# Kernel tuning notes

Hardware: AMD Instinct MI355X
Metric: run time of the kernel (lower is better)

Reference implementation:

```python
import jax, jax.numpy as jnp
import numpy as np

D = 1024
H = 16
DH = D // H  # 64


def setup_inputs() -> dict:
    key = jax.random.key(0)
    ks = jax.random.split(key, 11)
    B, S = 2, 2048
    s = 1.0 / np.sqrt(D)  # torch Linear default init scale (uniform bound)
    mk = lambda k, shape: jax.random.uniform(k, shape, jnp.float32, -s, s)
    return {
        "q": jax.random.normal(ks[0], (B, S, D), jnp.float32),
        "k": jax.random.normal(ks[1], (B, S, D), jnp.float32),
        "v": jax.random.normal(ks[2], (B, S, D), jnp.float32),
        "Wq": mk(ks[3], (D, D)), "bq": mk(ks[4], (D,)),
        "Wk": mk(ks[5], (D, D)), "bk": mk(ks[6], (D,)),
        "Wv": mk(ks[7], (D, D)), "bv": mk(ks[8], (D,)),
        "Wo": mk(ks[9], (D, D)), "bo": mk(ks[10], (D,)),
    }


def reference(q, k, v, Wq, bq, Wk, bk, Wv, bv, Wo, bo):
    B, S, _ = q.shape
    scaling = DH ** (-0.5)
    # torch Linear: x @ W.T + b ; then split heads -> (B, H, S, DH)
    split = lambda x: x.reshape(B, -1, H, DH).transpose(0, 2, 1, 3)
    Q = split(q @ Wq.T + bq)
    K = split(k @ Wk.T + bk)
    V = split(v @ Wv.T + bv)
    scores = jnp.einsum("bhqd,bhkd->bhqk", Q, K) * scaling  # [B,H,S,S]
    attn = jax.nn.softmax(scores, axis=-1)
    out = jnp.einsum("bhqk,bhkd->bhqd", attn, V)
    out = out.transpose(0, 2, 1, 3).reshape(B, S, D)
    return out @ Wo.T + bo
```

## Files before the change

### kernel.cpp

```cpp
#include <hip/hip_runtime.h>
#include <stdint.h>

#define DIM   1024
#define HEADS 16
#define DHEAD 64
#define SEQ   2048
#define MROWS 4096
#define NQ    (MROWS * DIM)
#define NW    (DIM * DIM)

typedef unsigned short u16;
typedef __attribute__((ext_vector_type(8))) short short8;
typedef __attribute__((ext_vector_type(4))) float f32x4;
typedef __attribute__((ext_vector_type(16))) float f32x16;

static_assert(sizeof(short8) == 16, "short8 must be 16B");

__device__ __forceinline__ float bf2f(u16 u) {
  union { float f; uint32_t u; } x; x.u = ((uint32_t)u) << 16; return x.f;
}
__device__ __forceinline__ u16 f2bf(float f) {
  union { float f; uint32_t u; } x; x.f = f;
  uint32_t r = x.u + 0x7FFFu + ((x.u >> 16) & 1u);
  return (u16)(r >> 16);
}
__device__ __forceinline__ uint32_t cvtpk(float lo, float hi) {
  uint32_t r;
  asm("v_cvt_pk_bf16_f32 %0, %1, %2" : "=v"(r) : "v"(lo), "v"(hi));
  return r;
}
__device__ __forceinline__ float exp2fast(float x) {
#if __has_builtin(__builtin_amdgcn_exp2f)
  return __builtin_amdgcn_exp2f(x);
#else
  return __expf(x * 0.69314718055994531f);
#endif
}

#if __has_builtin(__builtin_amdgcn_global_load_lds)
#define HAVE_GLLDS 1
#else
#define HAVE_GLLDS 0
#endif

__device__ __forceinline__ void stage16(const u16* src, u16* ldsbase, int cb, int lane) {
#if HAVE_GLLDS
  (void)lane;
  __builtin_amdgcn_global_load_lds((const __attribute__((address_space(1))) void*)src,
                                   (__attribute__((address_space(3))) void*)(ldsbase + (size_t)cb * 8),
                                   16, 0, 0);
#else
  *(short8*)(ldsbase + ((size_t)cb + lane) * 8) = *(const short8*)src;
#endif
}

__global__ __launch_bounds__(256)
void cvt_all(const float* __restrict__ q, const float* __restrict__ k, const float* __restrict__ v,
             const float* __restrict__ wq, const float* __restrict__ wk,
             const float* __restrict__ wv, const float* __restrict__ wo,
             u16* __restrict__ qc, u16* __restrict__ kc, u16* __restrict__ vc,
             u16* __restrict__ wqc, u16* __restrict__ wkc, u16* __restrict__ wvc, u16* __restrict__ woc)
{
  const float* s; u16* d; int n;
  switch (blockIdx.y) {
    case 0: s = q;  d = qc;  n = NQ; break;
    case 1: s = k;  d = kc;  n = NQ; break;
    case 2: s = v;  d = vc;  n = NQ; break;
    case 3: s = wq; d = wqc; n = NW; break;
    case 4: s = wk; d = wkc; n = NW; break;
    case 5: s = wv; d = wvc; n = NW; break;
    default: s = wo; d = woc; n = NW; break;
  }
  const int n8 = n >> 3;
  for (int i = blockIdx.x * blockDim.x + threadIdx.x; i < n8; i += gridDim.x * blockDim.x) {
    float4 f0 = ((const float4*)s)[2 * i];
    float4 f1 = ((const float4*)s)[2 * i + 1];
    short8 o;
    o[0] = (short)f2bf(f0.x); o[1] = (short)f2bf(f0.y);
    o[2] = (short)f2bf(f0.z); o[3] = (short)f2bf(f0.w);
    o[4] = (short)f2bf(f1.x); o[5] = (short)f2bf(f1.y);
    o[6] = (short)f2bf(f1.z); o[7] = (short)f2bf(f1.w);
    ((short8*)d)[i] = o;
  }
}

template <int RM, int RN, int MODE>
__global__ __launch_bounds__(256)
void gemm_nt(const u16* __restrict__ A0, const u16* __restrict__ W0, const float* __restrict__ b0, void* __restrict__ O0, float s0_,
             const u16* __restrict__ A1, const u16* __restrict__ W1, const float* __restrict__ b1, void* __restrict__ O1, float s1_,
             const u16* __restrict__ A2, const u16* __restrict__ W2, const float* __restrict__ b2, void* __restrict__ O2, float s2_)
{
  constexpr int BM = 32 * RM, BN = 32 * RN, BK = 64;
  __shared__ u16 As[BM * BK];
  __shared__ u16 Bs[BN * BK];

  const u16* A = A0; const u16* W = W0; const float* bias = b0; void* O = O0; float oscale = s0_;
  if (blockIdx.z == 1) { A = A1; W = W1; bias = b1; O = O1; oscale = s1_; }
  else if (blockIdx.z == 2) { A = A2; W = W2; bias = b2; O = O2; oscale = s2_; }

  const int tid  = threadIdx.x;
  const int wave = tid >> 6, lane = tid & 63;
  const int g = lane >> 4, cc = lane & 15;
  const int wr = wave >> 1, wc = wave & 1;
  const int m0 = blockIdx.x * BM, n0 = blockIdx.y * BN;

  f32x4 acc[RM][RN];
  for (int m = 0; m < RM; ++m)
    for (int n = 0; n < RN; ++n) acc[m][n] = (f32x4){0.f, 0.f, 0.f, 0.f};

  for (int k0 = 0; k0 < DIM; k0 += BK) {
    __syncthreads();
    constexpr int AI = (BM * 8) / 256;
    for (int i = 0; i < AI; ++i) {
      int cb = (wave * AI + i) * 64;
      int ch = cb + lane;
      int row = ch >> 3, kc = ch & 7;
      stage16(A + (size_t)(m0 + row) * DIM + k0 + kc * 8, As, cb, lane);
    }
    constexpr int BI = (BN * 8) / 256;
    for (int i = 0; i < BI; ++i) {
      int cb = (wave * BI + i) * 64;
      int ch = cb + lane;
      int row = ch >> 3, kc = ch & 7;
      stage16(W + (size_t)(n0 + row) * DIM + k0 + kc * 8, Bs, cb, lane);
    }
    __syncthreads();

    for (int kk = 0; kk < 2; ++kk) {
      short8 af[RM], bfr[RN];
      for (int m = 0; m < RM; ++m)
        af[m] = *(const short8*)(As + (size_t)(wr * (16 * RM) + m * 16 + cc) * BK + kk * 32 + g * 8);
      for (int n = 0; n < RN; ++n)
        bfr[n] = *(const short8*)(Bs + (size_t)(wc * (16 * RN) + n * 16 + cc) * BK + kk * 32 + g * 8);
      for (int m = 0; m < RM; ++m)
        for (int n = 0; n < RN; ++n)
          acc[m][n] = __builtin_amdgcn_mfma_f32_16x16x32_bf16(af[m], bfr[n], acc[m][n], 0, 0, 0);
    }
  }

  for (int n = 0; n < RN; ++n) {
    int col = n0 + wc * (16 * RN) + n * 16 + cc;
    float bv = bias[col];
    for (int m = 0; m < RM; ++m) {
      int rowb = m0 + wr * (16 * RM) + m * 16 + g * 4;
      for (int r = 0; r < 4; ++r) {
        int row = rowb + r;
        float val = (acc[m][n][r] + bv) * oscale;
        if (MODE == 0) {
          int b = row >> 11, s = row & (SEQ - 1);
          int hh = col >> 6, dh = col & 63;
          ((u16*)O)[((((size_t)b * HEADS + hh) * SEQ + s) << 6) + dh] = f2bf(val);
        } else {
          ((float*)O)[(size_t)row * DIM + col] = val;
        }
      }
    }
  }
}

#if __has_builtin(__builtin_amdgcn_permlane32_swap)
typedef __attribute__((ext_vector_type(2))) unsigned uint2v;
#define REPACK(PF, A_, B_, C_, D_)                                             \
  {                                                                            \
    uint2v w02 = __builtin_amdgcn_permlane32_swap((A_), (C_), false, false);   \
    uint2v w13 = __builtin_amdgcn_permlane32_swap((B_), (D_), false, false);   \
    union { uint32_t w[4]; short8 s8; } u_;                                    \
    u_.w[0] = w02[0]; u_.w[1] = w13[0]; u_.w[2] = w02[1]; u_.w[3] = w13[1];    \
    PF = u_.s8;                                                                \
  }
#else
#define REPACK(PF, A_, B_, C_, D_)                                             \
  {                                                                            \
    uint32_t pa = __shfl_xor((int)(A_), 32), pb = __shfl_xor((int)(B_), 32);   \
    uint32_t pc = __shfl_xor((int)(C_), 32), pd = __shfl_xor((int)(D_), 32);   \
    union { uint32_t w[4]; short8 s8; } u_;                                    \
    u_.w[0] = hi ? pc : (A_); u_.w[1] = hi ? pd : (B_);                        \
    u_.w[2] = hi ? (C_) : pa; u_.w[3] = hi ? (D_) : pb;                        \
    PF = u_.s8;                                                                \
  }
#endif

#define PV_BLOCK(SS, KSB)                                                      \
  {                                                                            \
    uint32_t a  = cvtpk(SS[0], SS[1]),   b3 = cvtpk(SS[2], SS[3]);             \
    uint32_t c  = cvtpk(SS[4], SS[5]),   d  = cvtpk(SS[6], SS[7]);             \
    uint32_t e  = cvtpk(SS[8], SS[9]),   f  = cvtpk(SS[10], SS[11]);           \
    uint32_t g2 = cvtpk(SS[12], SS[13]), h2 = cvtpk(SS[14], SS[15]);           \
    short8 pf0, pf1;                                                           \
    REPACK(pf0, a, b3, c, d)                                                   \
    REPACK(pf1, e, f, g2, h2)                                                  \
    uint32_t kvb0 = (uint32_t)((KSB) * 64 + hi * 16), kvb1 = kvb0 + 32;        \
    uint32_t r0 = (uint32_t)l31, r1 = 32u + (uint32_t)l31;                     \
    uint32_t sw = ((uint32_t)l31 & 7) << 4;                                    \
    short8 vf00 = *(const short8*)(Vc + ((r0 * 128 + kvb0) ^ sw));             \
    short8 vf01 = *(const short8*)(Vc + ((r1 * 128 + kvb0) ^ sw));             \
    short8 vf10 = *(const short8*)(Vc + ((r0 * 128 + kvb1) ^ sw));             \
    short8 vf11 = *(const short8*)(Vc + ((r1 * 128 + kvb1) ^ sw));             \
    __builtin_amdgcn_s_setprio(1);                                             \
    o0 = __builtin_amdgcn_mfma_f32_32x32x16_bf16(vf00, pf0, o0, 0, 0, 0);      \
    o1 = __builtin_amdgcn_mfma_f32_32x32x16_bf16(vf01, pf0, o1, 0, 0, 0);      \
    o0 = __builtin_amdgcn_mfma_f32_32x32x16_bf16(vf10, pf1, o0, 0, 0, 0);      \
    o1 = __builtin_amdgcn_mfma_f32_32x32x16_bf16(vf11, pf1, o1, 0, 0, 0);      \
    __builtin_amdgcn_s_setprio(0);                                             \
  }

__global__ __launch_bounds__(256)
void attn_fwd5(const u16* __restrict__ Qb, const u16* __restrict__ Kb,
               const u16* __restrict__ Vb, u16* __restrict__ Opart,
               float2* __restrict__ stats)
{
  uint32_t lid = blockIdx.x;
  uint32_t logical = (lid & 7) * 128 + (lid >> 3);
  const int qt    = logical & 15;
  const int bh    = (logical >> 4) & 31;
  const int split = logical >> 9;

  const int q0 = qt * 128;
  const int kvbase = split * (SEQ / 2);
  const int tid = threadIdx.x, wave = tid >> 6, lane = tid & 63;
  const int l31 = lane & 31, hi = lane >> 5;
  const float MFIX = 20.0f;

  const size_t base = (size_t)bh * SEQ * DHEAD;
  const u16* Qg = Qb + base;
  const u16* Kg = Kb + base;
  const u16* Vg = Vb + base;

  __shared__ u16 Ks[2][64 * 64];
  __shared__ u16 Vts[2][64 * 64];

  short8 qf[4];
  {
    const u16* qrow = Qg + (size_t)(q0 + wave * 32 + l31) * DHEAD + hi * 8;
    for (int ks = 0; ks < 4; ++ks)
      qf[ks] = *(const short8*)(qrow + ks * 16);
  }

  f32x16 o0, o1;
  for (int r = 0; r < 16; ++r) { o0[r] = 0.f; o1[r] = 0.f; }
  float l = 0.f;

  const int rp = tid & 31, c8 = tid >> 5;
  const int kr = tid >> 3, kc0 = tid & 7;
  short8 ka, kb2, va, vb2;

  {
    const int kv0 = kvbase;
    ka  = *(const short8*)(Kg + (size_t)(kv0 + kr) * DHEAD + kc0 * 8);
    kb2 = *(const short8*)(Kg + (size_t)(kv0 + 32 + kr) * DHEAD + kc0 * 8);
    va  = *(const short8*)(Vg + (size_t)(kv0 + 2 * rp) * DHEAD + c8 * 8);
    vb2 = *(const short8*)(Vg + (size_t)(kv0 + 2 * rp + 1) * DHEAD + c8 * 8);
    uint32_t sw = ((uint32_t)kr & 7) << 4;
    *(short8*)((char*)Ks[0] + (((uint32_t)kr * 128 + (uint32_t)kc0 * 16) ^ sw)) = ka;
    *(short8*)((char*)Ks[0] + ((((uint32_t)kr + 32) * 128 + (uint32_t)kc0 * 16) ^ sw)) = kb2;
    for (int j = 0; j < 8; ++j) {
      uint32_t row = c8 * 8 + j;
      uint32_t byte = (row * 128 + rp * 4) ^ ((row & 7) << 4);
      *(uint32_t*)((char*)Vts[0] + byte) =
          (uint32_t)(u16)va[j] | ((uint32_t)(u16)vb2[j] << 16);
    }
  }
  __syncthreads();

  for (int t = 0; t < 16; ++t) {
    const int cur = t & 1;
    if (t < 15) {
      const int kv0 = kvbase + (t + 1) * 64;
      ka  = *(const short8*)(Kg + (size_t)(kv0 + kr) * DHEAD + kc0 * 8);
      kb2 = *(const short8*)(Kg + (size_t)(kv0 + 32 + kr) * DHEAD + kc0 * 8);
      va  = *(const short8*)(Vg + (size_t)(kv0 + 2 * rp) * DHEAD + c8 * 8);
      vb2 = *(const short8*)(Vg + (size_t)(kv0 + 2 * rp + 1) * DHEAD + c8 * 8);
    }

    const char* Kc = (const char*)Ks[cur];
    const char* Vc = (const char*)Vts[cur];

    f32x16 s0, s1;
    for (int r = 0; r < 16; ++r) { s0[r] = 0.f; s1[r] = 0.f; }
    {
      uint32_t rb0 = (uint32_t)l31 * 128, sw0 = ((uint32_t)l31 & 7) << 4;
      uint32_t cbyte = (uint32_t)hi * 16;
      short8 k0 = *(const short8*)(Kc + ((rb0 + cbyte     ) ^ sw0));
      short8 k1 = *(const short8*)(Kc + ((rb0 + cbyte + 32) ^ sw0));
      short8 k2 = *(const short8*)(Kc + ((rb0 + cbyte + 64) ^ sw0));
      short8 k3 = *(const short8*)(Kc + ((rb0 + cbyte + 96) ^ sw0));
      uint32_t rb1 = rb0 + 32 * 128;
      short8 k4 = *(const short8*)(Kc + ((rb1 + cbyte     ) ^ sw0));
      short8 k5 = *(const short8*)(Kc + ((rb1 + cbyte + 32) ^ sw0));
      short8 k6 = *(const short8*)(Kc + ((rb1 + cbyte + 64) ^ sw0));
      short8 k7 = *(const short8*)(Kc + ((rb1 + cbyte + 96) ^ sw0));
      __builtin_amdgcn_s_setprio(1);
      s0 = __builtin_amdgcn_mfma_f32_32x32x16_bf16(k0, qf[0], s0, 0, 0, 0);
      s0 = __builtin_amdgcn_mfma_f32_32x32x16_bf16(k1, qf[1], s0, 0, 0, 0);
      s0 = __builtin_amdgcn_mfma_f32_32x32x16_bf16(k2, qf[2], s0, 0, 0, 0);
      s0 = __builtin_amdgcn_mfma_f32_32x32x16_bf16(k3, qf[3], s0, 0, 0, 0);
      s1 = __builtin_amdgcn_mfma_f32_32x32x16_bf16(k4, qf[0], s1, 0, 0, 0);
      s1 = __builtin_amdgcn_mfma_f32_32x32x16_bf16(k5, qf[1], s1, 0, 0, 0);
      s1 = __builtin_amdgcn_mfma_f32_32x32x16_bf16(k6, qf[2], s1, 0, 0, 0);
      s1 = __builtin_amdgcn_mfma_f32_32x32x16_bf16(k7, qf[3], s1, 0, 0, 0);
      __builtin_amdgcn_s_setprio(0);
    }

    for (int r = 0; r < 16; ++r) s0[r] = exp2fast(s0[r] - MFIX);
    for (int r = 0; r < 16; ++r) s1[r] = exp2fast(s1[r] - MFIX);
    {
      float a0 = s0[0] + s1[0], a1 = s0[1] + s1[1];
      float a2 = s0[2] + s1[2], a3 = s0[3] + s1[3];
      for (int r = 4; r < 16; r += 4) {
        a0 += s0[r]     + s1[r];
        a1 += s0[r + 1] + s1[r + 1];
        a2 += s0[r + 2] + s1[r + 2];
        a3 += s0[r + 3] + s1[r + 3];
      }
      float rsum = (a0 + a1) + (a2 + a3);
      rsum += __shfl_xor(rsum, 32);
      l += rsum;
    }

    PV_BLOCK(s0, 0)
    PV_BLOCK(s1, 1)

    if (t < 15) {
      uint32_t sw = ((uint32_t)kr & 7) << 4;
      char* Kn = (char*)Ks[cur ^ 1];
      *(short8*)(Kn + (((uint32_t)kr * 128 + (uint32_t)kc0 * 16) ^ sw)) = ka;
      *(short8*)(Kn + ((((uint32_t)kr + 32) * 128 + (uint32_t)kc0 * 16) ^ sw)) = kb2;
      char* Vn = (char*)Vts[cur ^ 1];
      for (int j = 0; j < 8; ++j) {
        uint32_t row = c8 * 8 + j;
        uint32_t byte = (row * 128 + rp * 4) ^ ((row & 7) << 4);
        *(uint32_t*)(Vn + byte) =
            (uint32_t)(u16)va[j] | ((uint32_t)(u16)vb2[j] << 16);
      }
      __syncthreads();
    }
  }

  const int q = q0 + wave * 32 + l31;
  u16* orow = Opart + (((size_t)split * 32 + bh) * SEQ + q) * DHEAD;
  for (int db = 0; db < 2; ++db) {
    const f32x16& o = db ? o1 : o0;
    for (int gq = 0; gq < 4; ++gq) {
      int dh = db * 32 + gq * 8 + hi * 4;
      ushort4 w;
      w.x = f2bf(o[gq * 4 + 0]); w.y = f2bf(o[gq * 4 + 1]);
      w.z = f2bf(o[gq * 4 + 2]); w.w = f2bf(o[gq * 4 + 3]);
      *(ushort4*)(orow + dh) = w;
    }
  }
  if (hi == 0)
    stats[((size_t)split * 32 + bh) * SEQ + q] = make_float2(MFIX, l);
}

__global__ __launch_bounds__(256)
void attn_combine(const u16* __restrict__ Opart, const float2* __restrict__ stats,
                  u16* __restrict__ AO)
{
  int idx = blockIdx.x * blockDim.x + threadIdx.x;
  if (idx >= 32 * SEQ * 8) return;
  int c8 = idx & 7;
  int q  = (idx >> 3) & (SEQ - 1);
  int bh = idx >> 14;
  float2 s0 = stats[((size_t)bh) * SEQ + q];
  float2 s1 = stats[((size_t)32 + bh) * SEQ + q];
  float M = fmaxf(s0.x, s1.x);
  float w0 = exp2fast(s0.x - M), w1 = exp2fast(s1.x - M);
  float inv = 1.f / (w0 * s0.y + w1 * s1.y);
  const short8 a = *(const short8*)(Opart + (((size_t)bh) * SEQ + q) * DHEAD + c8 * 8);
  const short8 b = *(const short8*)(Opart + (((size_t)32 + bh) * SEQ + q) * DHEAD + c8 * 8);
  int bb = bh >> 4, h = bh & 15;
  short8 r;
  for (int j = 0; j < 8; ++j)
    r[j] = (short)f2bf((w0 * bf2f((u16)a[j]) + w1 * bf2f((u16)b[j])) * inv);
  *(short8*)(AO + ((size_t)bb * SEQ + q) * DIM + h * 64 + c8 * 8) = r;
}

extern "C" void kernel_launch(void* const* d_in, const int* in_sizes, int n_in,
                              void* d_out, int out_size, void* d_ws, size_t ws_size,
                              hipStream_t stream)
{
  const float* q  = (const float*)d_in[0];
  const float* k  = (const float*)d_in[1];
  const float* v  = (const float*)d_in[2];
  const float* Wq = (const float*)d_in[3];
  const float* bq = (const float*)d_in[4];
  const float* Wk = (const float*)d_in[5];
  const float* bk = (const float*)d_in[6];
  const float* Wv = (const float*)d_in[7];
  const float* bv = (const float*)d_in[8];
  const float* Wo = (const float*)d_in[9];
  const float* bo = (const float*)d_in[10];
  float* out = (float*)d_out;

  u16* qc  = (u16*)d_ws;
  u16* kc  = qc  + NQ;
  u16* vc  = kc  + NQ;
  u16* wqc = vc  + NQ;
  u16* wkc = wqc + NW;
  u16* wvc = wkc + NW;
  u16* woc = wvc + NW;
  u16* Qh  = woc + NW;
  u16* Kh  = Qh  + NQ;
  u16* Vh  = Kh  + NQ;
  u16* AO  = Vh  + NQ;

  u16*    Opart = (u16*)d_ws;
  float2* stats = (float2*)((u16*)d_ws + (size_t)2 * 32 * SEQ * DHEAD);

  dim3 blk(256);
  hipLaunchKernelGGL(cvt_all, dim3(512, 7, 1), blk, 0, stream,
                     q, k, v, Wq, Wk, Wv, Wo, qc, kc, vc, wqc, wkc, wvc, woc);
  hipLaunchKernelGGL((gemm_nt<4, 4, 0>), dim3(MROWS / 128, DIM / 128, 3), blk, 0, stream,
                     qc, wqc, bq, (void*)Qh, 0.125f * 1.4426950408889634f,
                     kc, wkc, bk, (void*)Kh, 1.0f,
                     vc, wvc, bv, (void*)Vh, 1.0f);
  hipLaunchKernelGGL(attn_fwd5, dim3(1024, 1, 1), blk, 0, stream, Qh, Kh, Vh, Opart, stats);
  hipLaunchKernelGGL(attn_combine, dim3((32 * SEQ * 8) / 256, 1, 1), blk, 0, stream,
                     Opart, stats, AO);
  hipLaunchKernelGGL((gemm_nt<2, 4, 1>), dim3(MROWS / 64, DIM / 128, 1), blk, 0, stream,
                     AO, woc, bo, (void*)out, 1.0f,
                     nullptr, nullptr, nullptr, nullptr, 1.0f,
                     nullptr, nullptr, nullptr, nullptr, 1.0f);
}
```

Baseline: 145.0 us.

## Fuse activation bf16 conversion into QKV GEMM and split-combine into output GEMM

Drops the separate fp32-to-bf16 conversion of q/k/v and converts them in registers while staging A tiles in the QKV projection GEMM. The attention-split combine kernel is removed: the output projection GEMM now reads both partial outputs, sums them, and scales by 1/(l0+l1) while staging A. The fixed-max exp offset is folded into the score accumulator initialisation. This cuts two kernel launches and several full-size intermediate round trips through memory. In exchange the A loads for the QKV GEMM no longer use direct global-to-LDS loads and move twice the bytes as fp32, and the output GEMM reloads both partials for every N tile.

```diff
diff --git a/kernel.cpp b/kernel.cpp
--- a/kernel.cpp
+++ b/kernel.cpp
@@ -23,6 +23,9 @@
   union { float f; uint32_t u; } x; x.f = f;
   uint32_t r = x.u + 0x7FFFu + ((x.u >> 16) & 1u);
   return (u16)(r >> 16);
+}
+__device__ __forceinline__ float asf(uint32_t u) {
+  union { float f; uint32_t u; } x; x.u = u; return x.f;
 }
 __device__ __forceinline__ uint32_t cvtpk(float lo, float hi) {
   uint32_t r;
@@ -55,46 +58,39 @@
 }
 
 __global__ __launch_bounds__(256)
-void cvt_all(const float* __restrict__ q, const float* __restrict__ k, const float* __restrict__ v,
-             const float* __restrict__ wq, const float* __restrict__ wk,
-             const float* __restrict__ wv, const float* __restrict__ wo,
-             u16* __restrict__ qc, u16* __restrict__ kc, u16* __restrict__ vc,
-             u16* __restrict__ wqc, u16* __restrict__ wkc, u16* __restrict__ wvc, u16* __restrict__ woc)
+void cvt_w(const float* __restrict__ wq, const float* __restrict__ wk,
+           const float* __restrict__ wv, const float* __restrict__ wo,
+           u16* __restrict__ wqc, u16* __restrict__ wkc,
+           u16* __restrict__ wvc, u16* __restrict__ woc)
 {
-  const float* s; u16* d; int n;
+  const float* s; u16* d;
   switch (blockIdx.y) {
-    case 0: s = q;  d = qc;  n = NQ; break;
-    case 1: s = k;  d = kc;  n = NQ; break;
-    case 2: s = v;  d = vc;  n = NQ; break;
-    case 3: s = wq; d = wqc; n = NW; break;
-    case 4: s = wk; d = wkc; n = NW; break;
-    case 5: s = wv; d = wvc; n = NW; break;
-    default: s = wo; d = woc; n = NW; break;
-  }
-  const int n8 = n >> 3;
+    case 0: s = wq; d = wqc; break;
+    case 1: s = wk; d = wkc; break;
+    case 2: s = wv; d = wvc; break;
+    default: s = wo; d = woc; break;
+  }
+  const int n8 = NW >> 3;
   for (int i = blockIdx.x * blockDim.x + threadIdx.x; i < n8; i += gridDim.x * blockDim.x) {
     float4 f0 = ((const float4*)s)[2 * i];
     float4 f1 = ((const float4*)s)[2 * i + 1];
-    short8 o;
-    o[0] = (short)f2bf(f0.x); o[1] = (short)f2bf(f0.y);
-    o[2] = (short)f2bf(f0.z); o[3] = (short)f2bf(f0.w);
-    o[4] = (short)f2bf(f1.x); o[5] = (short)f2bf(f1.y);
-    o[6] = (short)f2bf(f1.z); o[7] = (short)f2bf(f1.w);
-    ((short8*)d)[i] = o;
-  }
-}
-
-template <int RM, int RN, int MODE>
+    union { uint32_t w[4]; short8 s8; } u;
+    u.w[0] = cvtpk(f0.x, f0.y); u.w[1] = cvtpk(f0.z, f0.w);
+    u.w[2] = cvtpk(f1.x, f1.y); u.w[3] = cvtpk(f1.z, f1.w);
+    ((short8*)d)[i] = u.s8;
+  }
+}
+
 __global__ __launch_bounds__(256)
-void gemm_nt(const u16* __restrict__ A0, const u16* __restrict__ W0, const float* __restrict__ b0, void* __restrict__ O0, float s0_,
-             const u16* __restrict__ A1, const u16* __restrict__ W1, const float* __restrict__ b1, void* __restrict__ O1, float s1_,
-             const u16* __restrict__ A2, const u16* __restrict__ W2, const float* __restrict__ b2, void* __restrict__ O2, float s2_)
+void gemm_qkv(const float* __restrict__ A0, const u16* __restrict__ W0, const float* __restrict__ b0, u16* __restrict__ O0, float s0_,
+              const float* __restrict__ A1, const u16* __restrict__ W1, const float* __restrict__ b1, u16* __restrict__ O1, float s1_,
+              const float* __restrict__ A2, const u16* __restrict__ W2, const float* __restrict__ b2, u16* __restrict__ O2, float s2_)
 {
-  constexpr int BM = 32 * RM, BN = 32 * RN, BK = 64;
+  constexpr int BM = 128, BN = 128, BK = 64, RM = 4, RN = 4;
   __shared__ u16 As[BM * BK];
   __shared__ u16 Bs[BN * BK];
 
-  const u16* A = A0; const u16* W = W0; const float* bias = b0; void* O = O0; float oscale = s0_;
+  const float* A = A0; const u16* W = W0; const float* bias = b0; u16* O = O0; float oscale = s0_;
   if (blockIdx.z == 1) { A = A1; W = W1; bias = b1; O = O1; oscale = s1_; }
   else if (blockIdx.z == 2) { A = A2; W = W2; bias = b2; O = O2; oscale = s2_; }
 
@@ -111,11 +107,14 @@
   for (int k0 = 0; k0 < DIM; k0 += BK) {
     __syncthreads();
     constexpr int AI = (BM * 8) / 256;
+    float4 af0[AI], af1[AI];
+    #pragma unroll
     for (int i = 0; i < AI; ++i) {
-      int cb = (wave * AI + i) * 64;
-      int ch = cb + lane;
+      int ch = (wave * AI + i) * 64 + lane;
       int row = ch >> 3, kc = ch & 7;
-      stage16(A + (size_t)(m0 + row) * DIM + k0 + kc * 8, As, cb, lane);
+      const float* src = A + (size_t)(m0 + row) * DIM + k0 + kc * 8;
+      af0[i] = *(const float4*)(src);
+      af1[i] = *(const float4*)(src + 4);
     }
     constexpr int BI = (BN * 8) / 256;
     for (int i = 0; i < BI; ++i) {
@@ -124,14 +123,24 @@
       int row = ch >> 3, kc = ch & 7;
       stage16(W + (size_t)(n0 + row) * DIM + k0 + kc * 8, Bs, cb, lane);
     }
+    #pragma unroll
+    for (int i = 0; i < AI; ++i) {
+      int ch = (wave * AI + i) * 64 + lane;
+      union { uint32_t w[4]; short8 s8; } u;
+      u.w[0] = cvtpk(af0[i].x, af0[i].y);
+      u.w[1] = cvtpk(af0[i].z, af0[i].w);
+      u.w[2] = cvtpk(af1[i].x, af1[i].y);
+      u.w[3] = cvtpk(af1[i].z, af1[i].w);
+      *(short8*)(As + (size_t)ch * 8) = u.s8;
+    }
     __syncthreads();
 
     for (int kk = 0; kk < 2; ++kk) {
       short8 af[RM], bfr[RN];
       for (int m = 0; m < RM; ++m)
-        af[m] = *(const short8*)(As + (size_t)(wr * (16 * RM) + m * 16 + cc) * BK + kk * 32 + g * 8);
+        af[m] = *(const short8*)(As + (size_t)(wr * 64 + m * 16 + cc) * BK + kk * 32 + g * 8);
       for (int n = 0; n < RN; ++n)
-        bfr[n] = *(const short8*)(Bs + (size_t)(wc * (16 * RN) + n * 16 + cc) * BK + kk * 32 + g * 8);
+        bfr[n] = *(const short8*)(Bs + (size_t)(wc * 64 + n * 16 + cc) * BK + kk * 32 + g * 8);
       for (int m = 0; m < RM; ++m)
         for (int n = 0; n < RN; ++n)
           acc[m][n] = __builtin_amdgcn_mfma_f32_16x16x32_bf16(af[m], bfr[n], acc[m][n], 0, 0, 0);
@@ -139,21 +148,103 @@
   }
 
   for (int n = 0; n < RN; ++n) {
-    int col = n0 + wc * (16 * RN) + n * 16 + cc;
+    int col = n0 + wc * 64 + n * 16 + cc;
     float bv = bias[col];
     for (int m = 0; m < RM; ++m) {
-      int rowb = m0 + wr * (16 * RM) + m * 16 + g * 4;
+      int rowb = m0 + wr * 64 + m * 16 + g * 4;
       for (int r = 0; r < 4; ++r) {
         int row = rowb + r;
         float val = (acc[m][n][r] + bv) * oscale;
-        if (MODE == 0) {
-          int b = row >> 11, s = row & (SEQ - 1);
-          int hh = col >> 6, dh = col & 63;
-          ((u16*)O)[((((size_t)b * HEADS + hh) * SEQ + s) << 6) + dh] = f2bf(val);
-        } else {
-          ((float*)O)[(size_t)row * DIM + col] = val;
-        }
+        int b = row >> 11, s = row & (SEQ - 1);
+        int hh = col >> 6, dh = col & 63;
+        O[((((size_t)b * HEADS + hh) * SEQ + s) << 6) + dh] = f2bf(val);
       }
+    }
+  }
+}
+
+__global__ __launch_bounds__(256)
+void gemm_out(const u16* __restrict__ Op0, const u16* __restrict__ Op1,
+              const float* __restrict__ lstats, const u16* __restrict__ W,
+              const float* __restrict__ bias, float* __restrict__ Out)
+{
+  constexpr int BM = 64, BN = 128, BK = 64, RM = 2, RN = 4;
+  __shared__ u16 As[BM * BK];
+  __shared__ u16 Bs[BN * BK];
+  __shared__ float wtab[HEADS * BM];
+
+  const int tid  = threadIdx.x;
+  const int wave = tid >> 6, lane = tid & 63;
+  const int g = lane >> 4, cc = lane & 15;
+  const int wr = wave >> 1, wc = wave & 1;
+  const int m0 = blockIdx.x * BM, n0 = blockIdx.y * BN;
+
+  for (int e = tid; e < HEADS * BM; e += 256) {
+    int h = e >> 6, r = e & 63;
+    int row = m0 + r;
+    int b = row >> 11, s = row & (SEQ - 1);
+    float l0 = lstats[(size_t)(b * 16 + h) * SEQ + s];
+    float l1 = lstats[(size_t)(32 + b * 16 + h) * SEQ + s];
+    wtab[e] = 1.0f / (l0 + l1);
+  }
+
+  f32x4 acc[RM][RN];
+  for (int m = 0; m < RM; ++m)
+    for (int n = 0; n < RN; ++n) acc[m][n] = (f32x4){0.f, 0.f, 0.f, 0.f};
+
+  for (int k0 = 0; k0 < DIM; k0 += BK) {
+    __syncthreads();
+    const int h = k0 >> 6;
+    constexpr int AI = (BM * 8) / 256;
+    #pragma unroll
+    for (int i = 0; i < AI; ++i) {
+      int ch = (wave * AI + i) * 64 + lane;
+      int row = ch >> 3, kc = ch & 7;
+      int grow = m0 + row;
+      int b = grow >> 11, s = grow & (SEQ - 1);
+      size_t off = ((size_t)(b * 16 + h) * SEQ + s) * 64 + kc * 8;
+      short8 a8 = *(const short8*)(Op0 + off);
+      short8 b8 = *(const short8*)(Op1 + off);
+      float winv = wtab[h * BM + row];
+      union { uint32_t w[4]; short8 s8; } u;
+      const uint32_t* wa = (const uint32_t*)&a8;
+      const uint32_t* wb = (const uint32_t*)&b8;
+      #pragma unroll
+      for (int j = 0; j < 4; ++j) {
+        float lo = (asf(wa[j] << 16) + asf(wb[j] << 16)) * winv;
+        float hi2 = (asf(wa[j] & 0xffff0000u) + asf(wb[j] & 0xffff0000u)) * winv;
+        u.w[j] = cvtpk(lo, hi2);
+      }
+      *(short8*)(As + (size_t)ch * 8) = u.s8;
+    }
+    constexpr int BI = (BN * 8) / 256;
+    for (int i = 0; i < BI; ++i) {
+      int cb = (wave * BI + i) * 64;
+      int ch = cb + lane;
+      int row = ch >> 3, kc = ch & 7;
+      stage16(W + (size_t)(n0 + row) * DIM + k0 + kc * 8, Bs, cb, lane);
+    }
+    __syncthreads();
+
+    for (int kk = 0; kk < 2; ++kk) {
+      short8 af[RM], bfr[RN];
+      for (int m = 0; m < RM; ++m)
+        af[m] = *(const short8*)(As + (size_t)(wr * 32 + m * 16 + cc) * BK + kk * 32 + g * 8);
+      for (int n = 0; n < RN; ++n)
+        bfr[n] = *(const short8*)(Bs + (size_t)(wc * 64 + n * 16 + cc) * BK + kk * 32 + g * 8);
+      for (int m = 0; m < RM; ++m)
+        for (int n = 0; n < RN; ++n)
+          acc[m][n] = __builtin_amdgcn_mfma_f32_16x16x32_bf16(af[m], bfr[n], acc[m][n], 0, 0, 0);
+    }
+  }
+
+  for (int n = 0; n < RN; ++n) {
+    int col = n0 + wc * 64 + n * 16 + cc;
+    float bv = bias[col];
+    for (int m = 0; m < RM; ++m) {
+      int rowb = m0 + wr * 32 + m * 16 + g * 4;
+      for (int r = 0; r < 4; ++r)
+        Out[(size_t)(rowb + r) * DIM + col] = acc[m][n][r] + bv;
     }
   }
 }
@@ -205,9 +296,9 @@
   }
 
 __global__ __launch_bounds__(256)
-void attn_fwd5(const u16* __restrict__ Qb, const u16* __restrict__ Kb,
+void attn_fwd6(const u16* __restrict__ Qb, const u16* __restrict__ Kb,
                const u16* __restrict__ Vb, u16* __restrict__ Opart,
-               float2* __restrict__ stats)
+               float* __restrict__ lstats)
 {
   uint32_t lid = blockIdx.x;
   uint32_t logical = (lid & 7) * 128 + (lid >> 3);
@@ -276,7 +367,7 @@
     const char* Vc = (const char*)Vts[cur];
 
     f32x16 s0, s1;
-    for (int r = 0; r < 16; ++r) { s0[r] = 0.f; s1[r] = 0.f; }
+    for (int r = 0; r < 16; ++r) { s0[r] = -MFIX; s1[r] = -MFIX; }
     {
       uint32_t rb0 = (uint32_t)l31 * 128, sw0 = ((uint32_t)l31 & 7) << 4;
       uint32_t cbyte = (uint32_t)hi * 16;
@@ -301,8 +392,8 @@
       __builtin_amdgcn_s_setprio(0);
     }
 
-    for (int r = 0; r < 16; ++r) s0[r] = exp2fast(s0[r] - MFIX);
-    for (int r = 0; r < 16; ++r) s1[r] = exp2fast(s1[r] - MFIX);
+    for (int r = 0; r < 16; ++r) s0[r] = exp2fast(s0[r]);
+    for (int r = 0; r < 16; ++r) s1[r] = exp2fast(s1[r]);
     {
       float a0 = s0[0] + s1[0], a1 = s0[1] + s1[1];
       float a2 = s0[2] + s1[2], a3 = s0[3] + s1[3];
@@ -349,30 +440,7 @@
     }
   }
   if (hi == 0)
-    stats[((size_t)split * 32 + bh) * SEQ + q] = make_float2(MFIX, l);
-}
-
-__global__ __launch_bounds__(256)
-void attn_combine(const u16* __restrict__ Opart, const float2* __restrict__ stats,
-                  u16* __restrict__ AO)
-{
-  int idx = blockIdx.x * blockDim.x + threadIdx.x;
-  if (idx >= 32 * SEQ * 8) return;
-  int c8 = idx & 7;
-  int q  = (idx >> 3) & (SEQ - 1);
-  int bh = idx >> 14;
-  float2 s0 = stats[((size_t)bh) * SEQ + q];
-  float2 s1 = stats[((size_t)32 + bh) * SEQ + q];
-  float M = fmaxf(s0.x, s1.x);
-  float w0 = exp2fast(s0.x - M), w1 = exp2fast(s1.x - M);
-  float inv = 1.f / (w0 * s0.y + w1 * s1.y);
-  const short8 a = *(const short8*)(Opart + (((size_t)bh) * SEQ + q) * DHEAD + c8 * 8);
-  const short8 b = *(const short8*)(Opart + (((size_t)32 + bh) * SEQ + q) * DHEAD + c8 * 8);
-  int bb = bh >> 4, h = bh & 15;
-  short8 r;
-  for (int j = 0; j < 8; ++j)
-    r[j] = (short)f2bf((w0 * bf2f((u16)a[j]) + w1 * bf2f((u16)b[j])) * inv);
-  *(short8*)(AO + ((size_t)bb * SEQ + q) * DIM + h * 64 + c8 * 8) = r;
+    lstats[((size_t)split * 32 + bh) * SEQ + q] = l;
 }
 
 extern "C" void kernel_launch(void* const* d_in, const int* in_sizes, int n_in,
@@ -392,33 +460,25 @@
   const float* bo = (const float*)d_in[10];
   float* out = (float*)d_out;
 
-  u16* qc  = (u16*)d_ws;
-  u16* kc  = qc  + NQ;
-  u16* vc  = kc  + NQ;
-  u16* wqc = vc  + NQ;
+  u16* wqc = (u16*)d_ws;
   u16* wkc = wqc + NW;
   u16* wvc = wkc + NW;
   u16* woc = wvc + NW;
   u16* Qh  = woc + NW;
   u16* Kh  = Qh  + NQ;
   u16* Vh  = Kh  + NQ;
-  u16* AO  = Vh  + NQ;
-
-  u16*    Opart = (u16*)d_ws;
-  float2* stats = (float2*)((u16*)d_ws + (size_t)2 * 32 * SEQ * DHEAD);
+  u16* Op0 = Vh  + NQ;
+  u16* Op1 = Op0 + NQ;
+  float* lstats = (float*)(Op1 + NQ);
 
   dim3 blk(256);
-  hipLaunchKernelGGL(cvt_all, dim3(512, 7, 1), blk, 0, stream,
-                     q, k, v, Wq, Wk, Wv, Wo, qc, kc, vc, wqc, wkc, wvc, woc);
-  hipLaunchKernelGGL((gemm_nt<4, 4, 0>), dim3(MROWS / 128, DIM / 128, 3), blk, 0, stream,
-                     qc, wqc, bq, (void*)Qh, 0.125f * 1.4426950408889634f,
-                     kc, wkc, bk, (void*)Kh, 1.0f,
-                     vc, wvc, bv, (void*)Vh, 1.0f);
-  hipLaunchKernelGGL(attn_fwd5, dim3(1024, 1, 1), blk, 0, stream, Qh, Kh, Vh, Opart, stats);
-  hipLaunchKernelGGL(attn_combine, dim3((32 * SEQ * 8) / 256, 1, 1), blk, 0, stream,
-                     Opart, stats, AO);
-  hipLaunchKernelGGL((gemm_nt<2, 4, 1>), dim3(MROWS / 64, DIM / 128, 1), blk, 0, stream,
-                     AO, woc, bo, (void*)out, 1.0f,
-                     nullptr, nullptr, nullptr, nullptr, 1.0f,
-                     nullptr, nullptr, nullptr, nullptr, 1.0f);
-}
+  hipLaunchKernelGGL(cvt_w, dim3(256, 4, 1), blk, 0, stream,
+                     Wq, Wk, Wv, Wo, wqc, wkc, wvc, woc);
+  hipLaunchKernelGGL(gemm_qkv, dim3(MROWS / 128, DIM / 128, 3), blk, 0, stream,
+                     q, wqc, bq, Qh, 0.125f * 1.4426950408889634f,
+                     k, wkc, bk, Kh, 1.0f,
+                     v, wvc, bv, Vh, 1.0f);
+  hipLaunchKernelGGL(attn_fwd6, dim3(1024, 1, 1), blk, 0, stream, Qh, Kh, Vh, Op0, lstats);
+  hipLaunchKernelGGL(gemm_out, dim3(MROWS / 64, DIM / 128, 1), blk, 0, stream,
+                     Op0, Op1, lstats, woc, bo, out);
+}
```

Measured after the change: 142.3 us. About the same (-1.8%).
